# Kernel optimization log

Measured on AMD Instinct MI355X. Metric: run time of the kernel, lower is better.

Reference implementation:

```python
import jax, jax.numpy as jnp
import numpy as np

D = 512
K = 14            # 13 anomaly classes + 1 normal
NORMAL_IDX = K - 1
ALPHA = 0.2       # PLG alpha
THETA = 0.55      # PLG threshold
EPS = 1e-8


def _minmax(x, axis):
    mn = jnp.min(x, axis=axis, keepdims=True)
    mx = jnp.max(x, axis=axis, keepdims=True)
    return (x - mn) / (mx - mn + EPS)


def setup_inputs() -> dict:
    key = jax.random.key(0)
    k1, k2, k3, k4, k5 = jax.random.split(key, 5)
    B_n, B_a, F = 16, 16, 4096
    normal_feats = jax.random.normal(k1, (B_n, F, D), dtype=jnp.float32)
    anomaly_feats = jax.random.normal(k2, (B_a, F, D), dtype=jnp.float32)
    anomaly_class_idx = jax.random.randint(k3, (B_a,), 0, K - 1)  # in [0, K-2]
    # learned text prompt embeddings (output of PromptTextEncoder, pre-normalization)
    T_emb = jax.random.normal(k4, (K, D), dtype=jnp.float32)
    # stand-in temporal scoring head (TCSAL replaced by linear head; see notes)
    w_score = jax.random.normal(k5, (D,), dtype=jnp.float32) / np.sqrt(D)
    b_score = jnp.zeros((), dtype=jnp.float32)
    return {"normal_feats": normal_feats, "anomaly_feats": anomaly_feats,
            "anomaly_class_idx": anomaly_class_idx, "T_emb": T_emb,
            "w_score": w_score, "b_score": b_score}


def reference(normal_feats, anomaly_feats, anomaly_class_idx, T_emb, w_score, b_score):
    B_a, F_a, _ = anomaly_feats.shape
    # L2-normalized text embeddings (K, D)
    T = T_emb / (jnp.linalg.norm(T_emb, axis=-1, keepdims=True) + EPS)
    T_anomaly = T[:NORMAL_IDX]          # (K-1, D)
    T_n = T[NORMAL_IDX]                 # (D,)  use_nvp=False -> T_n_enhanced = T_n
    T_n_enhanced = T_n

    # dense similarities
    S_nn = jnp.einsum('bfd,d->bf', normal_feats, T_n_enhanced)      # (B_n, F_n)
    phi_na = jnp.einsum('bfd,kd->bfk', normal_feats, T_anomaly)     # (B_n, F_n, K-1)
    S_an = jnp.einsum('bfd,d->bf', anomaly_feats, T_n_enhanced)     # (B_a, F_a)

    # per-sample true-class gather + matmul (vectorized: gather class vec then contract)
    T_true = T_anomaly[anomaly_class_idx]                            # (B_a, D)
    S_aa_true = jnp.einsum('bfd,bd->bf', anomaly_feats, T_true)      # (B_a, F_a)

    # 'other classes' similarities: exclude tau[b] per sample.
    # Since exactly one class is excluded, max_other = K-2 statically.
    phi_all = jnp.einsum('bfd,kd->bfk', anomaly_feats, T_anomaly)    # (B_a, F_a, K-1)
    j = jnp.arange(K - 2)                                            # (K-2,)
    other_idx = jnp.where(j[None, :] < anomaly_class_idx[:, None], j[None, :], j[None, :] + 1)  # (B_a, K-2)
    phi_aa_other = jnp.take_along_axis(
        phi_all, jnp.broadcast_to(other_idx[:, None, :], (B_a, F_a, K - 2)), axis=2)

    # pseudo-label generator (alpha-fused, normality-guided, thresholded)
    s_aa = _minmax(S_aa_true, axis=1)
    s_an = _minmax(S_an, axis=1)
    fused = (1.0 - ALPHA) * s_aa + ALPHA * (1.0 - s_an)
    pseudo_labels = (fused > THETA).astype(jnp.float32)

    # temporal scores (linear head stand-in for TCSAL)
    scores = jax.nn.sigmoid(jnp.einsum('bfd,d->bf', anomaly_feats, w_score) + b_score)

    S_aa_norm = _minmax(S_aa_true, axis=1)
    return (S_nn, phi_na, S_an, S_aa_true, phi_aa_other, S_aa_norm,
            pseudo_labels, scores, T_n_enhanced)
```

## Files before the change

kernel.cpp:

```cpp
#include <hip/hip_runtime.h>
#include <math.h>

#define D 512
#define K 14
#define EPS 1e-8f

#define O_SNN       0
#define O_PHINA     65536
#define O_SAN       917504
#define O_SAA       983040
#define O_PHIOTHER  1048576
#define O_SAANORM   1835008
#define O_PSEUDO    1900544
#define O_SCORES    1966080
#define O_TN        2031616

__device__ __forceinline__ float wave_sum(float v) {
    v += __shfl_xor(v, 1);
    v += __shfl_xor(v, 2);
    v += __shfl_xor(v, 4);
    v += __shfl_xor(v, 8);
    v += __shfl_xor(v, 16);
    v += __shfl_xor(v, 32);
    return v;
}
__device__ __forceinline__ float wave_min(float v) {
    v = fminf(v, __shfl_xor(v, 1));
    v = fminf(v, __shfl_xor(v, 2));
    v = fminf(v, __shfl_xor(v, 4));
    v = fminf(v, __shfl_xor(v, 8));
    v = fminf(v, __shfl_xor(v, 16));
    v = fminf(v, __shfl_xor(v, 32));
    return v;
}
__device__ __forceinline__ float wave_max(float v) {
    v = fmaxf(v, __shfl_xor(v, 1));
    v = fmaxf(v, __shfl_xor(v, 2));
    v = fmaxf(v, __shfl_xor(v, 4));
    v = fmaxf(v, __shfl_xor(v, 8));
    v = fmaxf(v, __shfl_xor(v, 16));
    v = fmaxf(v, __shfl_xor(v, 32));
    return v;
}

__device__ __forceinline__ float multi_reduce16(float (&vals)[16], int lane) {
#pragma unroll
    for (int s = 0; s < 4; s++) {
        const int half = 8 >> s;
        const bool sel = (lane >> s) & 1;
#pragma unroll
        for (int i = 0; i < half; i++) {
            float lo = vals[i], hi = vals[i + half];
            float a = sel ? lo : hi;
            float b = __shfl_xor(a, 1 << s);
            vals[i] = sel ? (hi + b) : (lo + b);
        }
    }
    float v = vals[0];
    v += __shfl_xor(v, 16);
    v += __shfl_xor(v, 32);
    return v;
}

__device__ __forceinline__ int bitrev4(int x) {
    return ((x & 1) << 3) | ((x & 2) << 1) | ((x & 4) >> 1) | ((x & 8) >> 3);
}

__global__ __launch_bounds__(960) void kprep(const float* __restrict__ T_emb,
                                             const float* __restrict__ w_score,
                                             float* __restrict__ W,
                                             float* __restrict__ tn_out) {
    int lane = threadIdx.x & 63;
    int w = threadIdx.x >> 6;
    float4* W4 = (float4*)W;
    if (w < K) {
        const float4* src = (const float4*)T_emb + w * 128;
        float4 a = src[lane];
        float4 b = src[64 + lane];
        float ss = a.x * a.x + a.y * a.y + a.z * a.z + a.w * a.w
                 + b.x * b.x + b.y * b.y + b.z * b.z + b.w * b.w;
        ss = wave_sum(ss);
        float inv = 1.0f / (sqrtf(ss) + EPS);
        float4 na = make_float4(a.x * inv, a.y * inv, a.z * inv, a.w * inv);
        float4 nb = make_float4(b.x * inv, b.y * inv, b.z * inv, b.w * inv);
        W4[w * 128 + lane] = na;
        W4[w * 128 + 64 + lane] = nb;
        if (w == K - 1) {
            float4* t4 = (float4*)tn_out;
            t4[lane] = na;
            t4[64 + lane] = nb;
        }
    } else {
        const float4* src = (const float4*)w_score;
        W4[14 * 128 + lane] = src[lane];
        W4[14 * 128 + 64 + lane] = src[64 + lane];
    }
}

__global__ __launch_bounds__(256, 2) void knormal(const float4* __restrict__ feats,
                                                  const float4* __restrict__ W4,
                                                  float* __restrict__ S_nn,
                                                  float* __restrict__ phi_na,
                                                  int nrows) {
    int lane = threadIdx.x & 63;
    int wave = (blockIdx.x * 256 + threadIdx.x) >> 6;
    int nwaves = (gridDim.x * 256) >> 6;

    float4 t0[K], t1[K];
#pragma unroll
    for (int k = 0; k < K; k++) {
        t0[k] = W4[k * 128 + lane];
        t1[k] = W4[k * 128 + 64 + lane];
    }
    const int myk = bitrev4(lane);

    int row = wave;
    float4 f0 = feats[row * 128 + lane];
    float4 f1 = feats[row * 128 + 64 + lane];
    while (row < nrows) {
        int nrow = row + nwaves;
        float4 g0, g1;
        if (nrow < nrows) {
            g0 = feats[nrow * 128 + lane];
            g1 = feats[nrow * 128 + 64 + lane];
        }
        float vals[16];
#pragma unroll
        for (int k = 0; k < K; k++) {
            vals[k] = f0.x * t0[k].x + f0.y * t0[k].y + f0.z * t0[k].z + f0.w * t0[k].w
                    + f1.x * t1[k].x + f1.y * t1[k].y + f1.z * t1[k].z + f1.w * t1[k].w;
        }
        vals[14] = 0.0f; vals[15] = 0.0f;
        float v = multi_reduce16(vals, lane);
        if (lane < 16 && myk < 14) {
            float* ptr = (myk < 13) ? (phi_na + row * 13 + myk) : (S_nn + row);
            *ptr = v;
        }
        row = nrow; f0 = g0; f1 = g1;
    }
}

__global__ __launch_bounds__(256, 2) void kanom(const float4* __restrict__ feats,
                                                const float4* __restrict__ W4,
                                                const int* __restrict__ cls,
                                                const float* __restrict__ b_score,
                                                float* __restrict__ S_an,
                                                float* __restrict__ S_aa,
                                                float* __restrict__ phi_other,
                                                float* __restrict__ scores,
                                                int nrows) {
    const int NK = 15;
    int lane = threadIdx.x & 63;
    int wave = (blockIdx.x * 256 + threadIdx.x) >> 6;
    int nwaves = (gridDim.x * 256) >> 6;

    float4 t0[NK], t1[NK];
#pragma unroll
    for (int k = 0; k < NK; k++) {
        t0[k] = W4[k * 128 + lane];
        t1[k] = W4[k * 128 + 64 + lane];
    }
    float bsc = *b_score;
    const int myk = bitrev4(lane);

    int row = wave;
    float4 f0 = feats[row * 128 + lane];
    float4 f1 = feats[row * 128 + 64 + lane];
    while (row < nrows) {
        int nrow = row + nwaves;
        float4 g0, g1;
        if (nrow < nrows) {
            g0 = feats[nrow * 128 + lane];
            g1 = feats[nrow * 128 + 64 + lane];
        }
        int ci = cls[row >> 12];
        float vals[16];
#pragma unroll
        for (int k = 0; k < NK; k++) {
            vals[k] = f0.x * t0[k].x + f0.y * t0[k].y + f0.z * t0[k].z + f0.w * t0[k].w
                    + f1.x * t1[k].x + f1.y * t1[k].y + f1.z * t1[k].z + f1.w * t1[k].w;
        }
        vals[15] = 0.0f;
        float v = multi_reduce16(vals, lane);
        if (lane < 16 && myk < 15) {
            float* ptr;
            float val = v;
            if (myk < 13) {
                if (myk == ci) ptr = S_aa + row;
                else           ptr = phi_other + row * 12 + ((myk < ci) ? myk : myk - 1);
            } else if (myk == 13) {
                ptr = S_an + row;
            } else {
                ptr = scores + row;
                val = 1.0f / (1.0f + expf(-(v + bsc)));
            }
            *ptr = val;
        }
        row = nrow; f0 = g0; f1 = g1;
    }
}

__global__ __launch_bounds__(256) void kminmax(const float* __restrict__ S_aa,
                                               const float* __restrict__ S_an,
                                               float* __restrict__ mm) {
    int b = blockIdx.x;
    int t = threadIdx.x;
    int lane = t & 63, wid = t >> 6;
    const float* pa = S_aa + b * 4096;
    const float* pn = S_an + b * 4096;
    float mnA = 1e30f, mxA = -1e30f, mnN = 1e30f, mxN = -1e30f;
    for (int i = t; i < 4096; i += 256) {
        float a = pa[i];
        float n = pn[i];
        mnA = fminf(mnA, a); mxA = fmaxf(mxA, a);
        mnN = fminf(mnN, n); mxN = fmaxf(mxN, n);
    }
    mnA = wave_min(mnA); mxA = wave_max(mxA);
    mnN = wave_min(mnN); mxN = wave_max(mxN);
    __shared__ float red[4][4];
    if (lane == 0) {
        red[wid][0] = mnA; red[wid][1] = mxA;
        red[wid][2] = mnN; red[wid][3] = mxN;
    }
    __syncthreads();
    if (t == 0) {
        float a0 = red[0][0], a1 = red[0][1], a2 = red[0][2], a3 = red[0][3];
        for (int w = 1; w < 4; w++) {
            a0 = fminf(a0, red[w][0]); a1 = fmaxf(a1, red[w][1]);
            a2 = fminf(a2, red[w][2]); a3 = fmaxf(a3, red[w][3]);
        }
        mm[b * 4 + 0] = a0; mm[b * 4 + 1] = a1;
        mm[b * 4 + 2] = a2; mm[b * 4 + 3] = a3;
    }
}

__global__ __launch_bounds__(256) void kfinal(const float* __restrict__ S_aa,
                                              const float* __restrict__ S_an,
                                              const float* __restrict__ mm,
                                              float* __restrict__ S_aa_norm,
                                              float* __restrict__ pseudo) {
    int i = blockIdx.x * 256 + threadIdx.x;
    if (i >= 65536) return;
    int b = i >> 12;
    float mnA = mm[b * 4 + 0], mxA = mm[b * 4 + 1];
    float mnN = mm[b * 4 + 2], mxN = mm[b * 4 + 3];
    float s_aa = (S_aa[i] - mnA) / (mxA - mnA + EPS);
    float s_an = (S_an[i] - mnN) / (mxN - mnN + EPS);
    float fused = 0.8f * s_aa + 0.2f * (1.0f - s_an);
    pseudo[i] = fused > 0.55f ? 1.0f : 0.0f;
    S_aa_norm[i] = s_aa;
}

extern "C" void kernel_launch(void* const* d_in, const int* in_sizes, int n_in,
                              void* d_out, int out_size, void* d_ws, size_t ws_size,
                              hipStream_t stream) {
    const float* normal_feats  = (const float*)d_in[0];
    const float* anomaly_feats = (const float*)d_in[1];
    const int*   cls           = (const int*)d_in[2];
    const float* T_emb         = (const float*)d_in[3];
    const float* w_score       = (const float*)d_in[4];
    const float* b_score       = (const float*)d_in[5];
    float* out = (float*)d_out;

    float* W  = (float*)d_ws;
    float* mm = (float*)d_ws + 15 * 512;

    const int nrows = 16 * 4096;

    kprep<<<1, 960, 0, stream>>>(T_emb, w_score, W, out + O_TN);

    knormal<<<1024, 256, 0, stream>>>((const float4*)normal_feats, (const float4*)W,
                                      out + O_SNN, out + O_PHINA, nrows);

    kanom<<<1024, 256, 0, stream>>>((const float4*)anomaly_feats, (const float4*)W,
                                    cls, b_score,
                                    out + O_SAN, out + O_SAA, out + O_PHIOTHER,
                                    out + O_SCORES, nrows);

    kminmax<<<16, 256, 0, stream>>>(out + O_SAA, out + O_SAN, mm);

    kfinal<<<256, 256, 0, stream>>>(out + O_SAA, out + O_SAN, mm,
                                    out + O_SAANORM, out + O_PSEUDO);
}
```

Before: 324.0 us.

## Fuse normal and anomaly projection kernels and merge min-max with finalize

Merges the two row-projection kernels into one launch that splits blocks between normal and anomaly features, and software-pipelines two rows per wave so the next row's load overlaps the current dot products and reduction. The min-max and normalization kernels are combined into one kernel that keeps values in registers. The prep kernel now runs as 15 single-wave blocks. This cuts launch count and tail idling and adds memory-level parallelism, at the cost of extra registers from the double-buffered values and a fixed row-count assumption.

```diff
diff --git a/kernel.cpp b/kernel.cpp
--- a/kernel.cpp
+++ b/kernel.cpp
@@ -4,6 +4,7 @@
 #define D 512
 #define K 14
 #define EPS 1e-8f
+#define NROWS 65536
 
 #define O_SNN       0
 #define O_PHINA     65536
@@ -66,12 +67,12 @@
     return ((x & 1) << 3) | ((x & 2) << 1) | ((x & 4) >> 1) | ((x & 8) >> 3);
 }
 
-__global__ __launch_bounds__(960) void kprep(const float* __restrict__ T_emb,
-                                             const float* __restrict__ w_score,
-                                             float* __restrict__ W,
-                                             float* __restrict__ tn_out) {
-    int lane = threadIdx.x & 63;
-    int w = threadIdx.x >> 6;
+__global__ __launch_bounds__(64) void kprep(const float* __restrict__ T_emb,
+                                            const float* __restrict__ w_score,
+                                            float* __restrict__ W,
+                                            float* __restrict__ tn_out) {
+    int lane = threadIdx.x;
+    int w = blockIdx.x;
     float4* W4 = (float4*)W;
     if (w < K) {
         const float4* src = (const float4*)T_emb + w * 128;
@@ -97,97 +98,41 @@
     }
 }
 
-__global__ __launch_bounds__(256, 2) void knormal(const float4* __restrict__ feats,
-                                                  const float4* __restrict__ W4,
-                                                  float* __restrict__ S_nn,
-                                                  float* __restrict__ phi_na,
-                                                  int nrows) {
-    int lane = threadIdx.x & 63;
-    int wave = (blockIdx.x * 256 + threadIdx.x) >> 6;
-    int nwaves = (gridDim.x * 256) >> 6;
-
-    float4 t0[K], t1[K];
-#pragma unroll
-    for (int k = 0; k < K; k++) {
-        t0[k] = W4[k * 128 + lane];
-        t1[k] = W4[k * 128 + 64 + lane];
-    }
-    const int myk = bitrev4(lane);
-
-    int row = wave;
-    float4 f0 = feats[row * 128 + lane];
-    float4 f1 = feats[row * 128 + 64 + lane];
-    while (row < nrows) {
-        int nrow = row + nwaves;
-        float4 g0, g1;
-        if (nrow < nrows) {
-            g0 = feats[nrow * 128 + lane];
-            g1 = feats[nrow * 128 + 64 + lane];
-        }
-        float vals[16];
-#pragma unroll
-        for (int k = 0; k < K; k++) {
-            vals[k] = f0.x * t0[k].x + f0.y * t0[k].y + f0.z * t0[k].z + f0.w * t0[k].w
-                    + f1.x * t1[k].x + f1.y * t1[k].y + f1.z * t1[k].z + f1.w * t1[k].w;
-        }
-        vals[14] = 0.0f; vals[15] = 0.0f;
-        float v = multi_reduce16(vals, lane);
-        if (lane < 16 && myk < 14) {
-            float* ptr = (myk < 13) ? (phi_na + row * 13 + myk) : (S_nn + row);
-            *ptr = v;
-        }
-        row = nrow; f0 = g0; f1 = g1;
-    }
-}
-
-__global__ __launch_bounds__(256, 2) void kanom(const float4* __restrict__ feats,
-                                                const float4* __restrict__ W4,
-                                                const int* __restrict__ cls,
-                                                const float* __restrict__ b_score,
-                                                float* __restrict__ S_an,
-                                                float* __restrict__ S_aa,
-                                                float* __restrict__ phi_other,
-                                                float* __restrict__ scores,
-                                                int nrows) {
-    const int NK = 15;
-    int lane = threadIdx.x & 63;
-    int wave = (blockIdx.x * 256 + threadIdx.x) >> 6;
-    int nwaves = (gridDim.x * 256) >> 6;
-
-    float4 t0[NK], t1[NK];
+template <int NK>
+__device__ __forceinline__ void dotvals(float (&vals)[16],
+                                        const float4 f0, const float4 f1,
+                                        const float4 (&t0)[NK], const float4 (&t1)[NK]) {
 #pragma unroll
     for (int k = 0; k < NK; k++) {
-        t0[k] = W4[k * 128 + lane];
-        t1[k] = W4[k * 128 + 64 + lane];
-    }
-    float bsc = *b_score;
-    const int myk = bitrev4(lane);
-
-    int row = wave;
-    float4 f0 = feats[row * 128 + lane];
-    float4 f1 = feats[row * 128 + 64 + lane];
-    while (row < nrows) {
-        int nrow = row + nwaves;
-        float4 g0, g1;
-        if (nrow < nrows) {
-            g0 = feats[nrow * 128 + lane];
-            g1 = feats[nrow * 128 + 64 + lane];
-        }
-        int ci = cls[row >> 12];
-        float vals[16];
-#pragma unroll
-        for (int k = 0; k < NK; k++) {
-            vals[k] = f0.x * t0[k].x + f0.y * t0[k].y + f0.z * t0[k].z + f0.w * t0[k].w
-                    + f1.x * t1[k].x + f1.y * t1[k].y + f1.z * t1[k].z + f1.w * t1[k].w;
-        }
-        vals[15] = 0.0f;
-        float v = multi_reduce16(vals, lane);
+        float s = f0.x * t0[k].x;
+        s = fmaf(f0.y, t0[k].y, s);
+        s = fmaf(f0.z, t0[k].z, s);
+        s = fmaf(f0.w, t0[k].w, s);
+        s = fmaf(f1.x, t1[k].x, s);
+        s = fmaf(f1.y, t1[k].y, s);
+        s = fmaf(f1.z, t1[k].z, s);
+        s = fmaf(f1.w, t1[k].w, s);
+        vals[k] = s;
+    }
+#pragma unroll
+    for (int k = NK; k < 16; k++) vals[k] = 0.0f;
+}
+
+template <bool ANOM>
+__device__ __forceinline__ void finish_row(float (&vals)[16], int row, int lane, int myk,
+                                           const int* __restrict__ cls, float bsc,
+                                           float* __restrict__ S_nn, float* __restrict__ phi_na,
+                                           float* __restrict__ S_an, float* __restrict__ S_aa,
+                                           float* __restrict__ phi_other, float* __restrict__ scores) {
+    float v = multi_reduce16(vals, lane);
+    if (ANOM) {
         if (lane < 16 && myk < 15) {
+            int ci = cls[row >> 12];
+            float val = v;
             float* ptr;
-            float val = v;
             if (myk < 13) {
-                if (myk == ci) ptr = S_aa + row;
-                else           ptr = phi_other + row * 12 + ((myk < ci) ? myk : myk - 1);
+                ptr = (myk == ci) ? (S_aa + row)
+                                  : (phi_other + row * 12 + ((myk < ci) ? myk : myk - 1));
             } else if (myk == 13) {
                 ptr = S_an + row;
             } else {
@@ -196,24 +141,104 @@
             }
             *ptr = val;
         }
-        row = nrow; f0 = g0; f1 = g1;
-    }
-}
-
-__global__ __launch_bounds__(256) void kminmax(const float* __restrict__ S_aa,
-                                               const float* __restrict__ S_an,
-                                               float* __restrict__ mm) {
+    } else {
+        if (lane < 16 && myk < 14) {
+            float* ptr = (myk < 13) ? (phi_na + row * 13 + myk) : (S_nn + row);
+            *ptr = v;
+        }
+    }
+}
+
+template <bool ANOM>
+__device__ __forceinline__ void run_half(const float4* __restrict__ feats,
+                                         const float4* __restrict__ W4,
+                                         const int* __restrict__ cls, float bsc,
+                                         int wave, int nw, int lane, int myk,
+                                         float* __restrict__ S_nn, float* __restrict__ phi_na,
+                                         float* __restrict__ S_an, float* __restrict__ S_aa,
+                                         float* __restrict__ phi_other, float* __restrict__ scores) {
+    constexpr int NK = ANOM ? 15 : 14;
+    float4 t0[NK], t1[NK];
+#pragma unroll
+    for (int k = 0; k < NK; k++) {
+        t0[k] = W4[k * 128 + lane];
+        t1[k] = W4[k * 128 + 64 + lane];
+    }
+
+    int pA = wave;
+    int pB = wave + nw;
+    int pC = wave + 2 * nw;
+
+    float4 A0 = feats[pA * 128 + lane];
+    float4 A1 = feats[pA * 128 + 64 + lane];
+    float4 B0 = feats[pB * 128 + lane];
+    float4 B1 = feats[pB * 128 + 64 + lane];
+    float valsA[16], valsB[16];
+    dotvals<NK>(valsA, A0, A1, t0, t1);
+
+    const int niter = NROWS / nw;
+#pragma unroll 1
+    for (int it = 0; it < (niter - 2) / 2; ++it) {
+        A0 = feats[pC * 128 + lane];
+        A1 = feats[pC * 128 + 64 + lane];
+        dotvals<NK>(valsB, B0, B1, t0, t1);
+        finish_row<ANOM>(valsA, pA, lane, myk, cls, bsc, S_nn, phi_na, S_an, S_aa, phi_other, scores);
+        pA = pB; pB = pC; pC += nw;
+        B0 = feats[pC * 128 + lane];
+        B1 = feats[pC * 128 + 64 + lane];
+        dotvals<NK>(valsA, A0, A1, t0, t1);
+        finish_row<ANOM>(valsB, pA, lane, myk, cls, bsc, S_nn, phi_na, S_an, S_aa, phi_other, scores);
+        pA = pB; pB = pC; pC += nw;
+    }
+    dotvals<NK>(valsB, B0, B1, t0, t1);
+    finish_row<ANOM>(valsA, pA, lane, myk, cls, bsc, S_nn, phi_na, S_an, S_aa, phi_other, scores);
+    finish_row<ANOM>(valsB, pB, lane, myk, cls, bsc, S_nn, phi_na, S_an, S_aa, phi_other, scores);
+}
+
+__global__ __launch_bounds__(256, 2) void kmain(const float4* __restrict__ nf,
+                                                const float4* __restrict__ af,
+                                                const float4* __restrict__ W4,
+                                                const int* __restrict__ cls,
+                                                const float* __restrict__ b_score,
+                                                float* __restrict__ S_nn,
+                                                float* __restrict__ phi_na,
+                                                float* __restrict__ S_an,
+                                                float* __restrict__ S_aa,
+                                                float* __restrict__ phi_other,
+                                                float* __restrict__ scores) {
+    int lane = threadIdx.x & 63;
+    int half = gridDim.x >> 1;
+    int nw = half << 2;
+    bool anom = (int)blockIdx.x >= half;
+    int bid = anom ? (int)blockIdx.x - half : (int)blockIdx.x;
+    int wave = (bid << 2) + (threadIdx.x >> 6);
+    int myk = bitrev4(lane);
+    float bsc = *b_score;
+    if (anom)
+        run_half<true>(af, W4, cls, bsc, wave, nw, lane, myk,
+                       S_nn, phi_na, S_an, S_aa, phi_other, scores);
+    else
+        run_half<false>(nf, W4, cls, bsc, wave, nw, lane, myk,
+                        S_nn, phi_na, S_an, S_aa, phi_other, scores);
+}
+
+__global__ __launch_bounds__(256) void kpost(const float* __restrict__ S_aa,
+                                             const float* __restrict__ S_an,
+                                             float* __restrict__ S_aa_norm,
+                                             float* __restrict__ pseudo) {
     int b = blockIdx.x;
     int t = threadIdx.x;
     int lane = t & 63, wid = t >> 6;
     const float* pa = S_aa + b * 4096;
     const float* pn = S_an + b * 4096;
+    float a[16], n[16];
     float mnA = 1e30f, mxA = -1e30f, mnN = 1e30f, mxN = -1e30f;
-    for (int i = t; i < 4096; i += 256) {
-        float a = pa[i];
-        float n = pn[i];
-        mnA = fminf(mnA, a); mxA = fmaxf(mxA, a);
-        mnN = fminf(mnN, n); mxN = fmaxf(mxN, n);
+#pragma unroll
+    for (int i = 0; i < 16; i++) {
+        a[i] = pa[t + i * 256];
+        n[i] = pn[t + i * 256];
+        mnA = fminf(mnA, a[i]); mxA = fmaxf(mxA, a[i]);
+        mnN = fminf(mnN, n[i]); mxN = fmaxf(mxN, n[i]);
     }
     mnA = wave_min(mnA); mxA = wave_max(mxA);
     mnN = wave_min(mnN); mxN = wave_max(mxN);
@@ -223,32 +248,20 @@
         red[wid][2] = mnN; red[wid][3] = mxN;
     }
     __syncthreads();
-    if (t == 0) {
-        float a0 = red[0][0], a1 = red[0][1], a2 = red[0][2], a3 = red[0][3];
-        for (int w = 1; w < 4; w++) {
-            a0 = fminf(a0, red[w][0]); a1 = fmaxf(a1, red[w][1]);
-            a2 = fminf(a2, red[w][2]); a3 = fmaxf(a3, red[w][3]);
-        }
-        mm[b * 4 + 0] = a0; mm[b * 4 + 1] = a1;
-        mm[b * 4 + 2] = a2; mm[b * 4 + 3] = a3;
-    }
-}
-
-__global__ __launch_bounds__(256) void kfinal(const float* __restrict__ S_aa,
-                                              const float* __restrict__ S_an,
-                                              const float* __restrict__ mm,
-                                              float* __restrict__ S_aa_norm,
-                                              float* __restrict__ pseudo) {
-    int i = blockIdx.x * 256 + threadIdx.x;
-    if (i >= 65536) return;
-    int b = i >> 12;
-    float mnA = mm[b * 4 + 0], mxA = mm[b * 4 + 1];
-    float mnN = mm[b * 4 + 2], mxN = mm[b * 4 + 3];
-    float s_aa = (S_aa[i] - mnA) / (mxA - mnA + EPS);
-    float s_an = (S_an[i] - mnN) / (mxN - mnN + EPS);
-    float fused = 0.8f * s_aa + 0.2f * (1.0f - s_an);
-    pseudo[i] = fused > 0.55f ? 1.0f : 0.0f;
-    S_aa_norm[i] = s_aa;
+    mnA = fminf(fminf(red[0][0], red[1][0]), fminf(red[2][0], red[3][0]));
+    mxA = fmaxf(fmaxf(red[0][1], red[1][1]), fmaxf(red[2][1], red[3][1]));
+    mnN = fminf(fminf(red[0][2], red[1][2]), fminf(red[2][2], red[3][2]));
+    mxN = fmaxf(fmaxf(red[0][3], red[1][3]), fmaxf(red[2][3], red[3][3]));
+    float dA = mxA - mnA + EPS;
+    float dN = mxN - mnN + EPS;
+#pragma unroll
+    for (int i = 0; i < 16; i++) {
+        float s_aa = (a[i] - mnA) / dA;
+        float s_an = (n[i] - mnN) / dN;
+        float fused = 0.8f * s_aa + 0.2f * (1.0f - s_an);
+        pseudo[b * 4096 + t + i * 256] = fused > 0.55f ? 1.0f : 0.0f;
+        S_aa_norm[b * 4096 + t + i * 256] = s_aa;
+    }
 }
 
 extern "C" void kernel_launch(void* const* d_in, const int* in_sizes, int n_in,
@@ -262,23 +275,16 @@
     const float* b_score       = (const float*)d_in[5];
     float* out = (float*)d_out;
 
-    float* W  = (float*)d_ws;
-    float* mm = (float*)d_ws + 15 * 512;
-
-    const int nrows = 16 * 4096;
-
-    kprep<<<1, 960, 0, stream>>>(T_emb, w_score, W, out + O_TN);
-
-    knormal<<<1024, 256, 0, stream>>>((const float4*)normal_feats, (const float4*)W,
-                                      out + O_SNN, out + O_PHINA, nrows);
-
-    kanom<<<1024, 256, 0, stream>>>((const float4*)anomaly_feats, (const float4*)W,
-                                    cls, b_score,
-                                    out + O_SAN, out + O_SAA, out + O_PHIOTHER,
-                                    out + O_SCORES, nrows);
-
-    kminmax<<<16, 256, 0, stream>>>(out + O_SAA, out + O_SAN, mm);
-
-    kfinal<<<256, 256, 0, stream>>>(out + O_SAA, out + O_SAN, mm,
-                                    out + O_SAANORM, out + O_PSEUDO);
-}
+    float* W = (float*)d_ws;
+
+    kprep<<<15, 64, 0, stream>>>(T_emb, w_score, W, out + O_TN);
+
+    kmain<<<2048, 256, 0, stream>>>((const float4*)normal_feats,
+                                    (const float4*)anomaly_feats,
+                                    (const float4*)W, cls, b_score,
+                                    out + O_SNN, out + O_PHINA, out + O_SAN, out + O_SAA,
+                                    out + O_PHIOTHER, out + O_SCORES);
+
+    kpost<<<16, 256, 0, stream>>>(out + O_SAA, out + O_SAN,
+                                  out + O_SAANORM, out + O_PSEUDO);
+}
```

New measurement: 361.7 us. 11.6% more time.
